# Performance work log

Measured on AMD Instinct MI355X. Metric: run time of the kernel, lower is better.

The kernel has to match this reference:

```python
import jax, jax.numpy as jnp
import numpy as np

B, H, W, K, PAD = 1024, 28, 28, 3, 1


def conv3x3(x, w, b):
    out = jax.lax.conv_general_dilated(x, w, (1, 1), ((PAD, PAD), (PAD, PAD)),
                                       dimension_numbers=('NCHW', 'OIHW', 'NCHW'))
    return out + b[None, :, None, None]


def deform_conv2d(x, offset, w, b):
    # torchvision deform_conv2d semantics, stride=1, pad=1, dilation=1, groups=1
    Bn, Cin, Hh, Ww = x.shape
    Cout = w.shape[0]
    KK = K * K
    off = offset.reshape(Bn, KK, 2, Hh, Ww)
    dy, dx = off[:, :, 0], off[:, :, 1]                      # [B,KK,H,W]
    ky, kx = jnp.meshgrid(jnp.arange(K, dtype=x.dtype), jnp.arange(K, dtype=x.dtype), indexing='ij')
    py = dy + (jnp.arange(Hh, dtype=x.dtype) - PAD)[None, None, :, None] + ky.reshape(KK)[None, :, None, None]
    px = dx + (jnp.arange(Ww, dtype=x.dtype) - PAD)[None, None, None, :] + kx.reshape(KK)[None, :, None, None]
    y0 = jnp.floor(py); x0 = jnp.floor(px)
    wy1 = py - y0; wy0 = 1.0 - wy1
    wx1 = px - x0; wx0 = 1.0 - wx1
    xf = x.reshape(Bn, Cin, Hh * Ww)

    def gather(yi, xi):
        valid = (yi >= 0) & (yi < Hh) & (xi >= 0) & (xi < Ww)
        yc = jnp.clip(yi, 0, Hh - 1).astype(jnp.int32)
        xc = jnp.clip(xi, 0, Ww - 1).astype(jnp.int32)
        idx = (yc * Ww + xc).reshape(Bn, -1)                 # [B, KK*H*W]
        g = jnp.take_along_axis(xf, jnp.broadcast_to(idx[:, None, :], (Bn, Cin, idx.shape[1])), axis=2)
        return g.reshape(Bn, Cin, KK, Hh, Ww) * valid.astype(x.dtype)[:, None]

    sampled = (gather(y0, x0) * (wy0 * wx0)[:, None]
               + gather(y0, x0 + 1) * (wy0 * wx1)[:, None]
               + gather(y0 + 1, x0) * (wy1 * wx0)[:, None]
               + gather(y0 + 1, x0 + 1) * (wy1 * wx1)[:, None])  # [B,Cin,KK,H,W]
    out = jnp.einsum('bkhw,ok->bohw', sampled.reshape(Bn, Cin * KK, Hh, Ww),
                     w.reshape(Cout, Cin * KK))
    return out + b[None, :, None, None]


def adaptive_avg_pool_14(x):
    Bn, C, Hh, Ww = x.shape
    f = Hh // 14
    return x.reshape(Bn, C, 14, f, 14, f).mean(axis=(3, 5))


def setup_inputs() -> dict:
    key = jax.random.key(0)
    ks = jax.random.split(key, 14)
    d = {}
    d['x'] = jax.random.normal(ks[0], (B, 1, H, W), dtype=jnp.float32)
    # offset conv 1: Conv2d(1, 18, 3, pad=1)
    d['ow1'] = jax.random.normal(ks[1], (18, 1, 3, 3), dtype=jnp.float32) * 0.1
    d['ob1'] = jnp.zeros((18,), jnp.float32)
    d['w1'] = jax.random.normal(ks[2], (32, 1, 3, 3), dtype=jnp.float32) * 0.01
    d['b1'] = jnp.zeros((32,), jnp.float32)
    # offset conv 2: Conv2d(32, 18, 3, pad=1)
    d['ow2'] = jax.random.normal(ks[3], (18, 32, 3, 3), dtype=jnp.float32) * 0.05
    d['ob2'] = jnp.zeros((18,), jnp.float32)
    d['w2'] = jax.random.normal(ks[4], (64, 32, 3, 3), dtype=jnp.float32) * 0.01
    d['b2'] = jnp.zeros((64,), jnp.float32)
    d['fw1'] = jax.random.normal(ks[5], (128, 64 * 14 * 14), dtype=jnp.float32) * 0.01
    d['fb1'] = jnp.zeros((128,), jnp.float32)
    d['fw2'] = jax.random.normal(ks[6], (10, 128), dtype=jnp.float32) * 0.05
    d['fb2'] = jnp.zeros((10,), jnp.float32)
    return d


def reference(x, ow1, ob1, w1, b1, ow2, ob2, w2, b2, fw1, fb1, fw2, fb2):
    # block1 + relu + pool 28->14
    h = deform_conv2d(x, conv3x3(x, ow1, ob1), w1, b1)
    h = adaptive_avg_pool_14(jax.nn.relu(h))
    # block2 + relu + pool 14->14 (identity)
    h = deform_conv2d(h, conv3x3(h, ow2, ob2), w2, b2)
    h = adaptive_avg_pool_14(jax.nn.relu(h))
    h = h.reshape(h.shape[0], -1)
    # classifier (ExcitationDropout is identity in eval mode)
    h = jax.nn.relu(h @ fw1.T + fb1)
    return h @ fw2.T + fb2
```

## Files before the change

kernel.cpp:

```cpp
#include <hip/hip_runtime.h>

#define NB 1024
#define TOTAL1 (NB*196)
#define SPS 200

#define WS_H1   0
#define WS_H2   6422528
#define WS_PART 19267584
#define WS_W1T  23461888
#define WS_OW1T 23462176
#define WS_W2T  23462338
#define WS_OW2T 23480770

__global__ __launch_bounds__(256) void prep(const float* __restrict__ w1,
                                            const float* __restrict__ ow1,
                                            const float* __restrict__ w2,
                                            const float* __restrict__ ow2,
                                            float* __restrict__ ws) {
  int i = blockIdx.x * 256 + threadIdx.x;
  if (i < 288)   { int co = i / 9,  kk = i % 9;   ws[WS_W1T  + kk * 32 + co] = w1[i]; }
  if (i < 162)   { int c  = i / 9,  j  = i % 9;   ws[WS_OW1T + j  * 18 + c ] = ow1[i]; }
  if (i < 18432) { int co = i / 288, k = i % 288; ws[WS_W2T  + k  * 64 + co] = w2[i]; }
  if (i < 5184)  { int c  = i / 288, k = i % 288; ws[WS_OW2T + k  * 18 + c ] = ow2[i]; }
}

__global__ __launch_bounds__(256, 2) void stage1(const float* __restrict__ x,
                                                 const float* __restrict__ ob1,
                                                 const float* __restrict__ b1,
                                                 const float* __restrict__ ws,
                                                 float* __restrict__ h1) {
  __shared__ float ximg[3 * 784];
  const float* __restrict__ w1t  = ws + WS_W1T;
  const float* __restrict__ ow1t = ws + WS_OW1T;
  int tid = threadIdx.x;
  int g0 = blockIdx.x * 256;
  int bfirst = g0 / 196;
  for (int idx = tid; idx < 3 * 784; idx += 256) {
    int img = idx / 784;
    int b = bfirst + img;
    ximg[idx] = (b < NB) ? x[b * 784 + (idx - img * 784)] : 0.f;
  }
  __syncthreads();
  int g = g0 + tid;
  if (g >= TOTAL1) return;
  int b = g / 196, p = g - b * 196;
  const float* im = ximg + (b - bfirst) * 784;
  int oy = p / 14, ox = p - (p / 14) * 14;

  float pooled[32];
#pragma unroll
  for (int co = 0; co < 32; ++co) pooled[co] = 0.f;

  for (int sub = 0; sub < 4; ++sub) {
    int y  = 2 * oy + (sub >> 1);
    int ix = 2 * ox + (sub & 1);
    float patch[9];
#pragma unroll
    for (int j = 0; j < 9; ++j) {
      int yy = y + j / 3 - 1, xc = ix + j % 3 - 1;
      bool ok = (yy >= 0) & (yy < 28) & (xc >= 0) & (xc < 28);
      patch[j] = ok ? im[yy * 28 + xc] : 0.f;
    }
    float off[18];
#pragma unroll
    for (int c = 0; c < 18; ++c) off[c] = ob1[c];
#pragma unroll
    for (int j = 0; j < 9; ++j) {
      float v = patch[j];
#pragma unroll
      for (int c = 0; c < 18; ++c) off[c] = fmaf(v, ow1t[j * 18 + c], off[c]);
    }
    float a[32];
#pragma unroll
    for (int co = 0; co < 32; ++co) a[co] = b1[co];
#pragma unroll
    for (int kk = 0; kk < 9; ++kk) {
      float py = (float)(y - 1 + kk / 3) + off[2 * kk];
      float px = (float)(ix - 1 + kk % 3) + off[2 * kk + 1];
      float y0f = floorf(py), x0f = floorf(px);
      float wy1 = py - y0f, wx1 = px - x0f;
      float wy0 = 1.f - wy1, wx0 = 1.f - wx1;
      int y0 = (int)y0f, x0 = (int)x0f;
      int y1 = y0 + 1, x1 = x0 + 1;
      bool vy0 = (y0 >= 0) & (y0 < 28), vy1 = (y1 >= 0) & (y1 < 28);
      bool vx0 = (x0 >= 0) & (x0 < 28), vx1 = (x1 >= 0) & (x1 < 28);
      float W00 = (vy0 & vx0) ? wy0 * wx0 : 0.f;
      float W01 = (vy0 & vx1) ? wy0 * wx1 : 0.f;
      float W10 = (vy1 & vx0) ? wy1 * wx0 : 0.f;
      float W11 = (vy1 & vx1) ? wy1 * wx1 : 0.f;
      int yc0 = min(max(y0, 0), 27), yc1 = min(max(y1, 0), 27);
      int xc0 = min(max(x0, 0), 27), xc1 = min(max(x1, 0), 27);
      float s = im[yc0 * 28 + xc0] * W00 + im[yc0 * 28 + xc1] * W01 +
                im[yc1 * 28 + xc0] * W10 + im[yc1 * 28 + xc1] * W11;
#pragma unroll
      for (int co = 0; co < 32; ++co) a[co] = fmaf(s, w1t[kk * 32 + co], a[co]);
    }
#pragma unroll
    for (int co = 0; co < 32; ++co) pooled[co] += fmaxf(a[co], 0.f);
  }
#pragma unroll
  for (int co = 0; co < 32; ++co) h1[b * 6272 + co * 196 + p] = pooled[co] * 0.25f;
}

__global__ __launch_bounds__(256, 3) void stage2(const float* __restrict__ h1,
                                                 const float* __restrict__ ob2,
                                                 const float* __restrict__ b2,
                                                 const float* __restrict__ ws,
                                                 float* __restrict__ h2) {
  __shared__ float imgT[196 * 32];
  __shared__ float Sbuf[32 * SPS + 8];
  __shared__ float offT[2 * 208];
  const float* __restrict__ w2t  = ws + WS_W2T;
  const float* __restrict__ ow2t = ws + WS_OW2T;
  int tid = threadIdx.x;
  int b = blockIdx.x;

  for (int e = tid; e < 6272; e += 256) {
    int ci = e / 196, p = e - ci * 196;
    imgT[p * 32 + ((ci + 4 * p) & 31)] = h1[b * 6272 + e];
  }

  int pp = tid;
  int spy = pp / 14, spx = pp - (pp / 14) * 14;

  int oc  = tid % 18;
  int opg = tid / 18;
  int op0 = opg * 16;
  bool oact = (tid < 234);
  float oacc[16];
#pragma unroll
  for (int i = 0; i < 16; ++i) oacc[i] = 0.f;

  for (int j = 0; j < 9; ++j) {
    __syncthreads();
    if (pp < 196) {
      int yy = spy + j / 3 - 1, xx = spx + j % 3 - 1;
      bool ok = (yy >= 0) & (yy < 14) & (xx >= 0) & (xx < 14);
      int idx = ok ? (yy * 14 + xx) : 0;
      const float* src = imgT + idx * 32;
      int rot = (4 * idx) & 31;
#pragma unroll
      for (int cg = 0; cg < 8; ++cg) {
        float4 v;
        if (ok) v = *(const float4*)(src + ((cg * 4 + rot) & 31));
        else    v = make_float4(0.f, 0.f, 0.f, 0.f);
        Sbuf[(cg * 4 + 0) * SPS + pp] = v.x;
        Sbuf[(cg * 4 + 1) * SPS + pp] = v.y;
        Sbuf[(cg * 4 + 2) * SPS + pp] = v.z;
        Sbuf[(cg * 4 + 3) * SPS + pp] = v.w;
      }
    } else if (pp < SPS) {
#pragma unroll
      for (int ci2 = 0; ci2 < 32; ++ci2) Sbuf[ci2 * SPS + pp] = 0.f;
    }
    __syncthreads();
    if (oact) {
      float wv[32];
#pragma unroll
      for (int ci2 = 0; ci2 < 32; ++ci2) wv[ci2] = ow2t[(ci2 * 9 + j) * 18 + oc];
      for (int ci2 = 0; ci2 < 32; ++ci2) {
        const float* srow = Sbuf + ci2 * SPS + op0;
        float w = wv[ci2];
#pragma unroll
        for (int t = 0; t < 4; ++t) {
          float4 s = *(const float4*)(srow + 4 * t);
          oacc[4 * t + 0] = fmaf(w, s.x, oacc[4 * t + 0]);
          oacc[4 * t + 1] = fmaf(w, s.y, oacc[4 * t + 1]);
          oacc[4 * t + 2] = fmaf(w, s.z, oacc[4 * t + 2]);
          oacc[4 * t + 3] = fmaf(w, s.w, oacc[4 * t + 3]);
        }
      }
    }
  }

  int cog = tid & 15, pg = tid >> 4;
  int co0 = cog * 4;
  int p0 = pg * 16;
  bool gact = (pg < 13);
  float acc[4][16];
  {
    float4 bb = *(const float4*)(b2 + co0);
    float bj[4] = {bb.x, bb.y, bb.z, bb.w};
#pragma unroll
    for (int jj = 0; jj < 4; ++jj)
#pragma unroll
      for (int i = 0; i < 16; ++i) acc[jj][i] = bj[jj];
  }
  float myob = oact ? ob2[oc] : 0.f;

  for (int kk = 0; kk < 9; ++kk) {
    __syncthreads();
    if (oact && (oc >> 1) == kk) {
      float* dst = offT + (oc & 1) * 208 + op0;
#pragma unroll
      for (int i = 0; i < 16; ++i) dst[i] = oacc[i] + myob;
    }
    __syncthreads();
    if (pp < 196) {
      float dyv = offT[pp];
      float dxv = offT[208 + pp];
      float pyv = (float)(spy - 1 + kk / 3) + dyv;
      float pxv = (float)(spx - 1 + kk % 3) + dxv;
      float y0f = floorf(pyv), x0f = floorf(pxv);
      float wy1 = pyv - y0f, wx1 = pxv - x0f;
      float wy0 = 1.f - wy1, wx0 = 1.f - wx1;
      int y0 = (int)y0f, x0 = (int)x0f;
      int y1 = y0 + 1, x1 = x0 + 1;
      bool vy0 = (y0 >= 0) & (y0 < 14), vy1 = (y1 >= 0) & (y1 < 14);
      bool vx0 = (x0 >= 0) & (x0 < 14), vx1 = (x1 >= 0) & (x1 < 14);
      float W00 = (vy0 & vx0) ? wy0 * wx0 : 0.f;
      float W01 = (vy0 & vx1) ? wy0 * wx1 : 0.f;
      float W10 = (vy1 & vx0) ? wy1 * wx0 : 0.f;
      float W11 = (vy1 & vx1) ? wy1 * wx1 : 0.f;
      int yc0 = min(max(y0, 0), 13), yc1 = min(max(y1, 0), 13);
      int xc0 = min(max(x0, 0), 13), xc1 = min(max(x1, 0), 13);
      int i00 = yc0 * 14 + xc0, i01 = yc0 * 14 + xc1;
      int i10 = yc1 * 14 + xc0, i11 = yc1 * 14 + xc1;
      const float* s00 = imgT + i00 * 32; int r00 = (4 * i00) & 31;
      const float* s01 = imgT + i01 * 32; int r01 = (4 * i01) & 31;
      const float* s10 = imgT + i10 * 32; int r10 = (4 * i10) & 31;
      const float* s11 = imgT + i11 * 32; int r11 = (4 * i11) & 31;
#pragma unroll
      for (int cg = 0; cg < 8; ++cg) {
        float4 a0 = *(const float4*)(s00 + ((cg * 4 + r00) & 31));
        float4 a1 = *(const float4*)(s01 + ((cg * 4 + r01) & 31));
        float4 a2 = *(const float4*)(s10 + ((cg * 4 + r10) & 31));
        float4 a3 = *(const float4*)(s11 + ((cg * 4 + r11) & 31));
        Sbuf[(cg * 4 + 0) * SPS + pp] = fmaf(W00, a0.x, fmaf(W01, a1.x, fmaf(W10, a2.x, W11 * a3.x)));
        Sbuf[(cg * 4 + 1) * SPS + pp] = fmaf(W00, a0.y, fmaf(W01, a1.y, fmaf(W10, a2.y, W11 * a3.y)));
        Sbuf[(cg * 4 + 2) * SPS + pp] = fmaf(W00, a0.z, fmaf(W01, a1.z, fmaf(W10, a2.z, W11 * a3.z)));
        Sbuf[(cg * 4 + 3) * SPS + pp] = fmaf(W00, a0.w, fmaf(W01, a1.w, fmaf(W10, a2.w, W11 * a3.w)));
      }
    } else if (pp < SPS) {
#pragma unroll
      for (int ci2 = 0; ci2 < 32; ++ci2) Sbuf[ci2 * SPS + pp] = 0.f;
    }
    __syncthreads();
    if (gact) {
      for (int cb = 0; cb < 32; cb += 4) {
        float4 w[4];
#pragma unroll
        for (int u = 0; u < 4; ++u)
          w[u] = *(const float4*)(w2t + ((cb + u) * 9 + kk) * 64 + co0);
#pragma unroll
        for (int u = 0; u < 4; ++u) {
          const float* srow = Sbuf + (cb + u) * SPS + p0;
          float4 s0 = *(const float4*)(srow);
          float4 s1 = *(const float4*)(srow + 4);
          float4 s2 = *(const float4*)(srow + 8);
          float4 s3 = *(const float4*)(srow + 12);
          float sv[16] = {s0.x, s0.y, s0.z, s0.w, s1.x, s1.y, s1.z, s1.w,
                          s2.x, s2.y, s2.z, s2.w, s3.x, s3.y, s3.z, s3.w};
          float wj[4] = {w[u].x, w[u].y, w[u].z, w[u].w};
#pragma unroll
          for (int jj = 0; jj < 4; ++jj)
#pragma unroll
            for (int i = 0; i < 16; ++i)
              acc[jj][i] = fmaf(wj[jj], sv[i], acc[jj][i]);
        }
      }
    }
  }

  if (gact) {
    float* __restrict__ orow = h2 + b * 12544 + co0 * 196 + p0;
#pragma unroll
    for (int jj = 0; jj < 4; ++jj) {
#pragma unroll
      for (int t = 0; t < 4; ++t) {
        if (p0 + 4 * t < 196) {
          float4 v;
          v.x = fmaxf(acc[jj][4 * t + 0], 0.f);
          v.y = fmaxf(acc[jj][4 * t + 1], 0.f);
          v.z = fmaxf(acc[jj][4 * t + 2], 0.f);
          v.w = fmaxf(acc[jj][4 * t + 3], 0.f);
          *(float4*)(orow + jj * 196 + 4 * t) = v;
        }
      }
    }
  }
}

__global__ __launch_bounds__(256, 2) void fc1(const float* __restrict__ h2,
                                              const float* __restrict__ fw1,
                                              float* __restrict__ part) {
  __shared__ float a_s[56 * 72];
  __shared__ float b_s[56 * 132];
  int tid = threadIdx.x;
  int rb = (blockIdx.x & 15) * 64;
  int ks = blockIdx.x >> 4;
  int kbase = ks * 392;
  int c0 = (tid & 31) * 4;
  int r0 = (tid >> 5) * 8;

  float acc[8][4];
#pragma unroll
  for (int i = 0; i < 8; ++i)
#pragma unroll
    for (int j = 0; j < 4; ++j) acc[i][j] = 0.f;

  for (int ch = 0; ch < 7; ++ch) {
    int kb = kbase + ch * 56;
    __syncthreads();
#pragma unroll
    for (int t = 0; t < 14; ++t) {
      int idx = t * 256 + tid;
      int r = idx / 56, k = idx - r * 56;
      a_s[k * 72 + r] = h2[(rb + r) * 12544 + kb + k];
    }
#pragma unroll
    for (int t = 0; t < 28; ++t) {
      int idx = t * 256 + tid;
      int c = idx / 56, k = idx - c * 56;
      b_s[k * 132 + c] = fw1[c * 12544 + kb + k];
    }
    __syncthreads();
    for (int k = 0; k < 56; ++k) {
      float4 bv = *(const float4*)&b_s[k * 132 + c0];
      float4 av0 = *(const float4*)&a_s[k * 72 + r0];
      float4 av1 = *(const float4*)&a_s[k * 72 + r0 + 4];
      float av[8] = {av0.x, av0.y, av0.z, av0.w, av1.x, av1.y, av1.z, av1.w};
      float bj[4] = {bv.x, bv.y, bv.z, bv.w};
#pragma unroll
      for (int i = 0; i < 8; ++i)
#pragma unroll
        for (int j = 0; j < 4; ++j) acc[i][j] = fmaf(av[i], bj[j], acc[i][j]);
    }
  }
#pragma unroll
  for (int i = 0; i < 8; ++i) {
    int r = rb + r0 + i;
#pragma unroll
    for (int j = 0; j < 4; ++j)
      part[(ks * 1024 + r) * 128 + c0 + j] = acc[i][j];
  }
}

__global__ __launch_bounds__(128) void fcfinal(const float* __restrict__ part,
                                               const float* __restrict__ fb1,
                                               const float* __restrict__ fw2,
                                               const float* __restrict__ fb2,
                                               float* __restrict__ out) {
  __shared__ float tbuf[128];
  int b = blockIdx.x, c = threadIdx.x;
  float s = fb1[c];
  for (int ks = 0; ks < 32; ++ks) s += part[(ks * 1024 + b) * 128 + c];
  tbuf[c] = fmaxf(s, 0.f);
  __syncthreads();
  if (c < 10) {
    float v = fb2[c];
#pragma unroll
    for (int k = 0; k < 128; ++k) v = fmaf(tbuf[k], fw2[c * 128 + k], v);
    out[b * 10 + c] = v;
  }
}

extern "C" void kernel_launch(void* const* d_in, const int* in_sizes, int n_in,
                              void* d_out, int out_size, void* d_ws, size_t ws_size,
                              hipStream_t stream) {
  const float* x   = (const float*)d_in[0];
  const float* ow1 = (const float*)d_in[1];
  const float* ob1 = (const float*)d_in[2];
  const float* w1  = (const float*)d_in[3];
  const float* b1  = (const float*)d_in[4];
  const float* ow2 = (const float*)d_in[5];
  const float* ob2 = (const float*)d_in[6];
  const float* w2  = (const float*)d_in[7];
  const float* b2  = (const float*)d_in[8];
  const float* fw1 = (const float*)d_in[9];
  const float* fb1 = (const float*)d_in[10];
  const float* fw2 = (const float*)d_in[11];
  const float* fb2 = (const float*)d_in[12];
  float* ws  = (float*)d_ws;
  float* out = (float*)d_out;

  prep<<<72, 256, 0, stream>>>(w1, ow1, w2, ow2, ws);
  stage1<<<784, 256, 0, stream>>>(x, ob1, b1, ws, ws + WS_H1);
  stage2<<<NB, 256, 0, stream>>>(ws + WS_H1, ob2, b2, ws, ws + WS_H2);
  fc1<<<512, 256, 0, stream>>>(ws + WS_H2, fw1, ws + WS_PART);
  fcfinal<<<1024, 128, 0, stream>>>(ws + WS_PART, fb1, fw2, fb2, out);
}
```

Before: 386.7 us.

## Restructure stage2 as one-thread-per-pixel with two images per block

The stage2 deformable-conv kernel is rewritten so each thread owns one output pixel. The thread computes all 18 offset channels and all 64 output channels in registers, reading weights directly from global/constant-like memory. This removes the shared staging buffer, the offset transpose and most block barriers, and packs two images into a 448-thread block. In exchange, each thread holds about 82 accumulators plus weight loads (risking register pressure and lower occupancy), does uniform-address weight loads per FMA, and writes outputs with strided scalar stores.

```diff
diff --git a/kernel.cpp b/kernel.cpp
--- a/kernel.cpp
+++ b/kernel.cpp
@@ -2,7 +2,6 @@
 
 #define NB 1024
 #define TOTAL1 (NB*196)
-#define SPS 200
 
 #define WS_H1   0
 #define WS_H2   6422528
@@ -102,182 +101,115 @@
   for (int co = 0; co < 32; ++co) h1[b * 6272 + co * 196 + p] = pooled[co] * 0.25f;
 }
 
-__global__ __launch_bounds__(256, 3) void stage2(const float* __restrict__ h1,
+__global__ __launch_bounds__(448, 4) void stage2(const float* __restrict__ h1,
                                                  const float* __restrict__ ob2,
                                                  const float* __restrict__ b2,
                                                  const float* __restrict__ ws,
                                                  float* __restrict__ h2) {
-  __shared__ float imgT[196 * 32];
-  __shared__ float Sbuf[32 * SPS + 8];
-  __shared__ float offT[2 * 208];
+  __shared__ float imgT[2 * 6272];
   const float* __restrict__ w2t  = ws + WS_W2T;
   const float* __restrict__ ow2t = ws + WS_OW2T;
   int tid = threadIdx.x;
-  int b = blockIdx.x;
-
-  for (int e = tid; e < 6272; e += 256) {
-    int ci = e / 196, p = e - ci * 196;
-    imgT[p * 32 + ((ci + 4 * p) & 31)] = h1[b * 6272 + e];
-  }
-
-  int pp = tid;
-  int spy = pp / 14, spx = pp - (pp / 14) * 14;
-
-  int oc  = tid % 18;
-  int opg = tid / 18;
-  int op0 = opg * 16;
-  bool oact = (tid < 234);
-  float oacc[16];
-#pragma unroll
-  for (int i = 0; i < 16; ++i) oacc[i] = 0.f;
-
+  int bb = blockIdx.x;
+
+  for (int e = tid; e < 12544; e += 448) {
+    int img = e / 6272, rem = e - img * 6272;
+    int ci = rem / 196, p = rem - ci * 196;
+    imgT[img * 6272 + p * 32 + ((ci + 4 * p) & 31)] = h1[bb * 12544 + e];
+  }
+  __syncthreads();
+
+  int img  = tid / 224;
+  int slot = tid - img * 224;
+  int py  = slot >> 4;
+  int pxc = slot & 15;
+  int pxx = min(pxc, 13);
+  int p   = py * 14 + pxx;
+  const float* im = imgT + img * 6272;
+
+  float off[18];
+#pragma unroll
+  for (int c = 0; c < 18; ++c) off[c] = ob2[c];
   for (int j = 0; j < 9; ++j) {
-    __syncthreads();
-    if (pp < 196) {
-      int yy = spy + j / 3 - 1, xx = spx + j % 3 - 1;
-      bool ok = (yy >= 0) & (yy < 14) & (xx >= 0) & (xx < 14);
-      int idx = ok ? (yy * 14 + xx) : 0;
-      const float* src = imgT + idx * 32;
-      int rot = (4 * idx) & 31;
-#pragma unroll
-      for (int cg = 0; cg < 8; ++cg) {
-        float4 v;
-        if (ok) v = *(const float4*)(src + ((cg * 4 + rot) & 31));
-        else    v = make_float4(0.f, 0.f, 0.f, 0.f);
-        Sbuf[(cg * 4 + 0) * SPS + pp] = v.x;
-        Sbuf[(cg * 4 + 1) * SPS + pp] = v.y;
-        Sbuf[(cg * 4 + 2) * SPS + pp] = v.z;
-        Sbuf[(cg * 4 + 3) * SPS + pp] = v.w;
+    int yy = py + j / 3 - 1, xx = pxx + j % 3 - 1;
+    bool ok = (yy >= 0) & (yy < 14) & (xx >= 0) & (xx < 14);
+    int nidx = ok ? (yy * 14 + xx) : 0;
+    const float* src = im + nidx * 32;
+    int rot = (4 * nidx) & 31;
+    for (int cq = 0; cq < 8; ++cq) {
+      float4 v;
+      if (ok) v = *(const float4*)(src + ((cq * 4 + rot) & 31));
+      else    v = make_float4(0.f, 0.f, 0.f, 0.f);
+      const float* w0 = ow2t + ((cq * 4 + 0) * 9 + j) * 18;
+      const float* w1 = ow2t + ((cq * 4 + 1) * 9 + j) * 18;
+      const float* w2 = ow2t + ((cq * 4 + 2) * 9 + j) * 18;
+      const float* w3 = ow2t + ((cq * 4 + 3) * 9 + j) * 18;
+#pragma unroll
+      for (int c = 0; c < 18; ++c) {
+        off[c] = fmaf(v.x, w0[c], off[c]);
+        off[c] = fmaf(v.y, w1[c], off[c]);
+        off[c] = fmaf(v.z, w2[c], off[c]);
+        off[c] = fmaf(v.w, w3[c], off[c]);
       }
-    } else if (pp < SPS) {
-#pragma unroll
-      for (int ci2 = 0; ci2 < 32; ++ci2) Sbuf[ci2 * SPS + pp] = 0.f;
-    }
-    __syncthreads();
-    if (oact) {
-      float wv[32];
-#pragma unroll
-      for (int ci2 = 0; ci2 < 32; ++ci2) wv[ci2] = ow2t[(ci2 * 9 + j) * 18 + oc];
-      for (int ci2 = 0; ci2 < 32; ++ci2) {
-        const float* srow = Sbuf + ci2 * SPS + op0;
-        float w = wv[ci2];
-#pragma unroll
-        for (int t = 0; t < 4; ++t) {
-          float4 s = *(const float4*)(srow + 4 * t);
-          oacc[4 * t + 0] = fmaf(w, s.x, oacc[4 * t + 0]);
-          oacc[4 * t + 1] = fmaf(w, s.y, oacc[4 * t + 1]);
-          oacc[4 * t + 2] = fmaf(w, s.z, oacc[4 * t + 2]);
-          oacc[4 * t + 3] = fmaf(w, s.w, oacc[4 * t + 3]);
-        }
+    }
+  }
+
+  float acc[64];
+#pragma unroll
+  for (int co = 0; co < 64; ++co) acc[co] = b2[co];
+
+  for (int kk = 0; kk < 9; ++kk) {
+    float dy = off[0], dx = off[1];
+#pragma unroll
+    for (int t = 1; t < 9; ++t) if (kk == t) { dy = off[2 * t]; dx = off[2 * t + 1]; }
+
+    float pyv = (float)(py - 1 + kk / 3) + dy;
+    float pxv = (float)(pxx - 1 + kk % 3) + dx;
+    float y0f = floorf(pyv), x0f = floorf(pxv);
+    float wy1 = pyv - y0f, wx1 = pxv - x0f;
+    float wy0 = 1.f - wy1, wx0 = 1.f - wx1;
+    int y0 = (int)y0f, x0 = (int)x0f;
+    int y1 = y0 + 1, x1 = x0 + 1;
+    bool vy0 = (y0 >= 0) & (y0 < 14), vy1 = (y1 >= 0) & (y1 < 14);
+    bool vx0 = (x0 >= 0) & (x0 < 14), vx1 = (x1 >= 0) & (x1 < 14);
+    float W00 = (vy0 & vx0) ? wy0 * wx0 : 0.f;
+    float W01 = (vy0 & vx1) ? wy0 * wx1 : 0.f;
+    float W10 = (vy1 & vx0) ? wy1 * wx0 : 0.f;
+    float W11 = (vy1 & vx1) ? wy1 * wx1 : 0.f;
+    int yc0 = min(max(y0, 0), 13), yc1 = min(max(y1, 0), 13);
+    int xc0 = min(max(x0, 0), 13), xc1 = min(max(x1, 0), 13);
+    int i00 = yc0 * 14 + xc0, i01 = yc0 * 14 + xc1;
+    int i10 = yc1 * 14 + xc0, i11 = yc1 * 14 + xc1;
+    int o00 = i00 * 32, r00 = (4 * i00) & 31;
+    int o01 = i01 * 32, r01 = (4 * i01) & 31;
+    int o10 = i10 * 32, r10 = (4 * i10) & 31;
+    int o11 = i11 * 32, r11 = (4 * i11) & 31;
+
+    for (int cq = 0; cq < 8; ++cq) {
+      float4 a0 = *(const float4*)(im + o00 + ((cq * 4 + r00) & 31));
+      float4 a1 = *(const float4*)(im + o01 + ((cq * 4 + r01) & 31));
+      float4 a2 = *(const float4*)(im + o10 + ((cq * 4 + r10) & 31));
+      float4 a3 = *(const float4*)(im + o11 + ((cq * 4 + r11) & 31));
+      float s0 = fmaf(W00, a0.x, fmaf(W01, a1.x, fmaf(W10, a2.x, W11 * a3.x)));
+      float s1 = fmaf(W00, a0.y, fmaf(W01, a1.y, fmaf(W10, a2.y, W11 * a3.y)));
+      float s2 = fmaf(W00, a0.z, fmaf(W01, a1.z, fmaf(W10, a2.z, W11 * a3.z)));
+      float s3 = fmaf(W00, a0.w, fmaf(W01, a1.w, fmaf(W10, a2.w, W11 * a3.w)));
+#pragma unroll
+      for (int u = 0; u < 4; ++u) {
+        float su = (u == 0) ? s0 : (u == 1) ? s1 : (u == 2) ? s2 : s3;
+        const float* wr = w2t + ((cq * 4 + u) * 9 + kk) * 64;
+#pragma unroll
+        for (int co = 0; co < 64; ++co)
+          acc[co] = fmaf(su, wr[co], acc[co]);
       }
     }
   }
 
-  int cog = tid & 15, pg = tid >> 4;
-  int co0 = cog * 4;
-  int p0 = pg * 16;
-  bool gact = (pg < 13);
-  float acc[4][16];
-  {
-    float4 bb = *(const float4*)(b2 + co0);
-    float bj[4] = {bb.x, bb.y, bb.z, bb.w};
-#pragma unroll
-    for (int jj = 0; jj < 4; ++jj)
-#pragma unroll
-      for (int i = 0; i < 16; ++i) acc[jj][i] = bj[jj];
-  }
-  float myob = oact ? ob2[oc] : 0.f;
-
-  for (int kk = 0; kk < 9; ++kk) {
-    __syncthreads();
-    if (oact && (oc >> 1) == kk) {
-      float* dst = offT + (oc & 1) * 208 + op0;
-#pragma unroll
-      for (int i = 0; i < 16; ++i) dst[i] = oacc[i] + myob;
-    }
-    __syncthreads();
-    if (pp < 196) {
-      float dyv = offT[pp];
-      float dxv = offT[208 + pp];
-      float pyv = (float)(spy - 1 + kk / 3) + dyv;
-      float pxv = (float)(spx - 1 + kk % 3) + dxv;
-      float y0f = floorf(pyv), x0f = floorf(pxv);
-      float wy1 = pyv - y0f, wx1 = pxv - x0f;
-      float wy0 = 1.f - wy1, wx0 = 1.f - wx1;
-      int y0 = (int)y0f, x0 = (int)x0f;
-      int y1 = y0 + 1, x1 = x0 + 1;
-      bool vy0 = (y0 >= 0) & (y0 < 14), vy1 = (y1 >= 0) & (y1 < 14);
-      bool vx0 = (x0 >= 0) & (x0 < 14), vx1 = (x1 >= 0) & (x1 < 14);
-      float W00 = (vy0 & vx0) ? wy0 * wx0 : 0.f;
-      float W01 = (vy0 & vx1) ? wy0 * wx1 : 0.f;
-      float W10 = (vy1 & vx0) ? wy1 * wx0 : 0.f;
-      float W11 = (vy1 & vx1) ? wy1 * wx1 : 0.f;
-      int yc0 = min(max(y0, 0), 13), yc1 = min(max(y1, 0), 13);
-      int xc0 = min(max(x0, 0), 13), xc1 = min(max(x1, 0), 13);
-      int i00 = yc0 * 14 + xc0, i01 = yc0 * 14 + xc1;
-      int i10 = yc1 * 14 + xc0, i11 = yc1 * 14 + xc1;
-      const float* s00 = imgT + i00 * 32; int r00 = (4 * i00) & 31;
-      const float* s01 = imgT + i01 * 32; int r01 = (4 * i01) & 31;
-      const float* s10 = imgT + i10 * 32; int r10 = (4 * i10) & 31;
-      const float* s11 = imgT + i11 * 32; int r11 = (4 * i11) & 31;
-#pragma unroll
-      for (int cg = 0; cg < 8; ++cg) {
-        float4 a0 = *(const float4*)(s00 + ((cg * 4 + r00) & 31));
-        float4 a1 = *(const float4*)(s01 + ((cg * 4 + r01) & 31));
-        float4 a2 = *(const float4*)(s10 + ((cg * 4 + r10) & 31));
-        float4 a3 = *(const float4*)(s11 + ((cg * 4 + r11) & 31));
-        Sbuf[(cg * 4 + 0) * SPS + pp] = fmaf(W00, a0.x, fmaf(W01, a1.x, fmaf(W10, a2.x, W11 * a3.x)));
-        Sbuf[(cg * 4 + 1) * SPS + pp] = fmaf(W00, a0.y, fmaf(W01, a1.y, fmaf(W10, a2.y, W11 * a3.y)));
-        Sbuf[(cg * 4 + 2) * SPS + pp] = fmaf(W00, a0.z, fmaf(W01, a1.z, fmaf(W10, a2.z, W11 * a3.z)));
-        Sbuf[(cg * 4 + 3) * SPS + pp] = fmaf(W00, a0.w, fmaf(W01, a1.w, fmaf(W10, a2.w, W11 * a3.w)));
-      }
-    } else if (pp < SPS) {
-#pragma unroll
-      for (int ci2 = 0; ci2 < 32; ++ci2) Sbuf[ci2 * SPS + pp] = 0.f;
-    }
-    __syncthreads();
-    if (gact) {
-      for (int cb = 0; cb < 32; cb += 4) {
-        float4 w[4];
-#pragma unroll
-        for (int u = 0; u < 4; ++u)
-          w[u] = *(const float4*)(w2t + ((cb + u) * 9 + kk) * 64 + co0);
-#pragma unroll
-        for (int u = 0; u < 4; ++u) {
-          const float* srow = Sbuf + (cb + u) * SPS + p0;
-          float4 s0 = *(const float4*)(srow);
-          float4 s1 = *(const float4*)(srow + 4);
-          float4 s2 = *(const float4*)(srow + 8);
-          float4 s3 = *(const float4*)(srow + 12);
-          float sv[16] = {s0.x, s0.y, s0.z, s0.w, s1.x, s1.y, s1.z, s1.w,
-                          s2.x, s2.y, s2.z, s2.w, s3.x, s3.y, s3.z, s3.w};
-          float wj[4] = {w[u].x, w[u].y, w[u].z, w[u].w};
-#pragma unroll
-          for (int jj = 0; jj < 4; ++jj)
-#pragma unroll
-            for (int i = 0; i < 16; ++i)
-              acc[jj][i] = fmaf(wj[jj], sv[i], acc[jj][i]);
-        }
-      }
-    }
-  }
-
-  if (gact) {
-    float* __restrict__ orow = h2 + b * 12544 + co0 * 196 + p0;
-#pragma unroll
-    for (int jj = 0; jj < 4; ++jj) {
-#pragma unroll
-      for (int t = 0; t < 4; ++t) {
-        if (p0 + 4 * t < 196) {
-          float4 v;
-          v.x = fmaxf(acc[jj][4 * t + 0], 0.f);
-          v.y = fmaxf(acc[jj][4 * t + 1], 0.f);
-          v.z = fmaxf(acc[jj][4 * t + 2], 0.f);
-          v.w = fmaxf(acc[jj][4 * t + 3], 0.f);
-          *(float4*)(orow + jj * 196 + 4 * t) = v;
-        }
-      }
-    }
+  if (pxc < 14) {
+    int base = (2 * bb + img) * 12544 + p;
+#pragma unroll
+    for (int co = 0; co < 64; ++co)
+      h2[base + co * 196] = fmaxf(acc[co], 0.f);
   }
 }
 
@@ -376,7 +308,7 @@
 
   prep<<<72, 256, 0, stream>>>(w1, ow1, w2, ow2, ws);
   stage1<<<784, 256, 0, stream>>>(x, ob1, b1, ws, ws + WS_H1);
-  stage2<<<NB, 256, 0, stream>>>(ws + WS_H1, ob2, b2, ws, ws + WS_H2);
+  stage2<<<512, 448, 0, stream>>>(ws + WS_H1, ob2, b2, ws, ws + WS_H2);
   fc1<<<512, 256, 0, stream>>>(ws + WS_H2, fw1, ws + WS_PART);
   fcfinal<<<1024, 128, 0, stream>>>(ws + WS_PART, fb1, fw2, fb2, out);
 }
```

Result: slower. 433.8 us (+12.2%).
